# Kernel optimization log

Hardware: AMD Instinct MI355X
Metric: run time of the kernel (lower is better)

## Reference

```python
import jax, jax.numpy as jnp
import numpy as np

N = 512        # number of evidences
D = 512        # hidden_dim

def setup_inputs() -> dict:
    key = jax.random.key(0)
    k0, k1, k2, k3, k4 = jax.random.split(key, 5)
    s = 1.0 / np.sqrt(2 * D)
    return {
        "h_e":  jax.random.normal(k0, (N, D), dtype=jnp.float32),
        "W0_w": jax.random.uniform(k1, (D, 2 * D), minval=-s, maxval=s, dtype=jnp.float32),  # nn.Linear(2d, d).weight
        "W0_b": jax.random.uniform(k2, (D,), minval=-s, maxval=s, dtype=jnp.float32),
        "W1_w": jax.random.uniform(k3, (1, D), minval=-1/np.sqrt(D), maxval=1/np.sqrt(D), dtype=jnp.float32),
        "W1_b": jax.random.uniform(k4, (1,), minval=-1/np.sqrt(D), maxval=1/np.sqrt(D), dtype=jnp.float32),
    }

def reference(h_e, W0_w, W0_b, W0b_unused=None, W1_w=None, W1_b=None):
    pass  # placeholder replaced below

def reference(h_e, W0_w, W0_b, W1_w, W1_b):
    d = h_e.shape[-1]
    # W_0([h_i ; h_j]) == h_i @ A^T + h_j @ B^T where W0_w = [A | B]
    Wa = W0_w[:, :d]          # [d, d] acts on h_i
    Wb = W0_w[:, d:]          # [d, d] acts on h_j
    pre_i = jnp.einsum('id,hd->ih', h_e, Wa)            # [n, d]
    pre_j = jnp.einsum('jd,hd->jh', h_e, Wb)            # [n, d]
    hidden = jax.nn.relu(pre_i[:, None, :] + pre_j[None, :, :] + W0_b)  # [n, n, d]
    p = jnp.einsum('ijh,oh->ijo', hidden, W1_w)[..., 0] + W1_b[0]       # [n, n]
    a = jax.nn.softmax(p, axis=-1)                                      # [n, n]
    return a @ h_e                                                      # [n, d]
```

## Files before the change

### kernel.cpp

```cpp
#include <hip/hip_runtime.h>


using bf16x8 = __attribute__((ext_vector_type(8))) short;
using f32x4  = __attribute__((ext_vector_type(4))) float;
using f16x2  = __attribute__((ext_vector_type(2))) _Float16;
using f16x4  = __attribute__((ext_vector_type(4))) _Float16;
using f16x8  = __attribute__((ext_vector_type(8))) _Float16;

#define SC_STR 68

__device__ __forceinline__ unsigned short f2bf(float x) {
    unsigned int u = __float_as_uint(x);
    u += 0x7fffu + ((u >> 16) & 1u);
    return (unsigned short)(u >> 16);
}

__device__ __forceinline__ unsigned short f2h(float x) {
    _Float16 h = (_Float16)x;
    union { _Float16 h; unsigned short u; } c; c.h = h;
    return c.u;
}

__global__ __launch_bounds__(256) void k_prep(const float* __restrict__ he,
                                              const float* __restrict__ w0,
                                              unsigned short* __restrict__ heb,
                                              _Float16* __restrict__ hebT,
                                              unsigned short* __restrict__ w0b) {
    const int tid = threadIdx.x;
    if (blockIdx.z == 0) {
        __shared__ unsigned short T[64][65];
        const int r0 = blockIdx.y * 64, c0 = blockIdx.x * 64;
        #pragma unroll
        for (int rep = 0; rep < 4; ++rep) {
            int f = tid + rep * 256;
            int row = f >> 4, col = (f & 15) * 4;
            float4 a = *(const float4*)&he[(r0 + row) * 512 + c0 + col];
            *(ushort4*)&heb[(r0 + row) * 512 + c0 + col] =
                make_ushort4(f2bf(a.x), f2bf(a.y), f2bf(a.z), f2bf(a.w));
            T[row][col + 0] = f2h(a.x); T[row][col + 1] = f2h(a.y);
            T[row][col + 2] = f2h(a.z); T[row][col + 3] = f2h(a.w);
        }
        __syncthreads();
        #pragma unroll
        for (int rep = 0; rep < 4; ++rep) {
            int f = tid + rep * 256;
            int trow = f >> 4, tcol = (f & 15) * 4;
            ushort4 v = make_ushort4(T[tcol + 0][trow], T[tcol + 1][trow],
                                     T[tcol + 2][trow], T[tcol + 3][trow]);
            *(ushort4*)&hebT[(c0 + trow) * 512 + r0 + tcol] = v;
        }
    } else {
        const int r0 = blockIdx.y * 64, c0 = blockIdx.x * 64 + (blockIdx.z - 1) * 512;
        #pragma unroll
        for (int rep = 0; rep < 4; ++rep) {
            int f = tid + rep * 256;
            int row = f >> 4, col = (f & 15) * 4;
            float4 a = *(const float4*)&w0[(r0 + row) * 1024 + c0 + col];
            *(ushort4*)&w0b[(r0 + row) * 1024 + c0 + col] =
                make_ushort4(f2bf(a.x), f2bf(a.y), f2bf(a.z), f2bf(a.w));
        }
    }
}

__global__ __launch_bounds__(64) void k_preA(const unsigned short* __restrict__ heb,
                                             const unsigned short* __restrict__ w0b,
                                             const float* __restrict__ b0,
                                             _Float16* __restrict__ CI,
                                             _Float16* __restrict__ CJ) {
    const int l = threadIdx.x;
    const int c0 = blockIdx.x * 32;
    const int i0 = blockIdx.y * 32;
    const int r16 = l & 15;
    const int k0l = (l >> 4) * 8;
    const int hrow0 = c0 & 511;
    const int dofs = (c0 >= 512) ? 512 : 0;

    f32x4 acc[2][2] = {};
    const unsigned short* pa0 = heb + (i0 + r16) * 512;
    const unsigned short* pa1 = heb + (i0 + 16 + r16) * 512;
    const unsigned short* pb0 = w0b + (hrow0 + r16) * 1024 + dofs;
    const unsigned short* pb1 = w0b + (hrow0 + 16 + r16) * 1024 + dofs;

    #pragma unroll
    for (int ks = 0; ks < 16; ++ks) {
        const int k0 = ks * 32 + k0l;
        bf16x8 a0 = *(const bf16x8*)(pa0 + k0);
        bf16x8 a1 = *(const bf16x8*)(pa1 + k0);
        bf16x8 b0v = *(const bf16x8*)(pb0 + k0);
        bf16x8 b1v = *(const bf16x8*)(pb1 + k0);
        acc[0][0] = __builtin_amdgcn_mfma_f32_16x16x32_bf16(a0, b0v, acc[0][0], 0, 0, 0);
        acc[0][1] = __builtin_amdgcn_mfma_f32_16x16x32_bf16(a0, b1v, acc[0][1], 0, 0, 0);
        acc[1][0] = __builtin_amdgcn_mfma_f32_16x16x32_bf16(a1, b0v, acc[1][0], 0, 0, 0);
        acc[1][1] = __builtin_amdgcn_mfma_f32_16x16x32_bf16(a1, b1v, acc[1][1], 0, 0, 0);
    }
    const int orow = (l >> 4) * 4;
    if (dofs) {
        const float bb0 = b0[hrow0 + r16];
        const float bb1 = b0[hrow0 + 16 + r16];
        #pragma unroll
        for (int ti = 0; ti < 2; ++ti)
            #pragma unroll
            for (int tj = 0; tj < 2; ++tj) {
                const float bb = tj ? bb1 : bb0;
                #pragma unroll
                for (int r = 0; r < 4; ++r)
                    CJ[(i0 + ti * 16 + orow + r) * 512 + hrow0 + tj * 16 + r16] =
                        (_Float16)(acc[ti][tj][r] + bb);
            }
    } else {
        #pragma unroll
        for (int ti = 0; ti < 2; ++ti)
            #pragma unroll
            for (int tj = 0; tj < 2; ++tj)
                #pragma unroll
                for (int r = 0; r < 4; ++r)
                    CI[(i0 + ti * 16 + orow + r) * 512 + c0 + tj * 16 + r16] =
                        (_Float16)acc[ti][tj][r];
    }
}

__global__ __launch_bounds__(256) void k_score(const _Float16* __restrict__ CI,
                                               const _Float16* __restrict__ CJ,
                                               const float* __restrict__ w1,
                                               _Float16* __restrict__ Ppart) {
    const int tid = threadIdx.x;
    const int tx = tid & 15, ty = tid >> 4;
    const int j0 = blockIdx.x * 64;
    const int i0 = blockIdx.y * 64;
    const int hs = blockIdx.z;

    __shared__ __align__(16) f16x2 As2[16 * SC_STR];
    __shared__ __align__(16) f16x2 Bs2[16 * SC_STR];
    __shared__ f16x2 Ws2[16];

    const f16x2 fz = {(_Float16)0, (_Float16)0};
    float acc[4][4] = {};

    for (int kt = 0; kt < 2; ++kt) {
        const int hb = hs * 64 + kt * 32;
        {
            const int row = tid >> 2;
            const int hc = (tid & 3) * 8;
            const int hp = hc >> 1;
            f16x8 av = *(const f16x8*)&CI[(i0 + row) * 512 + hb + hc];
            As2[(hp + 0) * SC_STR + row] = __builtin_shufflevector(av, av, 0, 1);
            As2[(hp + 1) * SC_STR + row] = __builtin_shufflevector(av, av, 2, 3);
            As2[(hp + 2) * SC_STR + row] = __builtin_shufflevector(av, av, 4, 5);
            As2[(hp + 3) * SC_STR + row] = __builtin_shufflevector(av, av, 6, 7);
            f16x8 bv = *(const f16x8*)&CJ[(j0 + row) * 512 + hb + hc];
            Bs2[(hp + 0) * SC_STR + row] = __builtin_shufflevector(bv, bv, 0, 1);
            Bs2[(hp + 1) * SC_STR + row] = __builtin_shufflevector(bv, bv, 2, 3);
            Bs2[(hp + 2) * SC_STR + row] = __builtin_shufflevector(bv, bv, 4, 5);
            Bs2[(hp + 3) * SC_STR + row] = __builtin_shufflevector(bv, bv, 6, 7);
        }
        if (tid < 16) {
            float2 w = *(const float2*)&w1[hb + 2 * tid];
            f16x2 wp = {(_Float16)w.x, (_Float16)w.y};
            Ws2[tid] = wp;
        }
        __syncthreads();
        #pragma unroll
        for (int k = 0; k < 16; ++k) {
            f16x8 a8 = *(const f16x8*)&As2[k * SC_STR + 4 * ty];
            f16x8 b8 = *(const f16x8*)&Bs2[k * SC_STR + 4 * tx];
            const f16x2 w = Ws2[k];
            f16x2 ap[4] = { __builtin_shufflevector(a8, a8, 0, 1),
                            __builtin_shufflevector(a8, a8, 2, 3),
                            __builtin_shufflevector(a8, a8, 4, 5),
                            __builtin_shufflevector(a8, a8, 6, 7) };
            f16x2 bp[4] = { __builtin_shufflevector(b8, b8, 0, 1),
                            __builtin_shufflevector(b8, b8, 2, 3),
                            __builtin_shufflevector(b8, b8, 4, 5),
                            __builtin_shufflevector(b8, b8, 6, 7) };
            #pragma unroll
            for (int ii = 0; ii < 4; ++ii)
                #pragma unroll
                for (int jj = 0; jj < 4; ++jj) {
                    f16x2 s = ap[ii] + bp[jj];
                    s = __builtin_elementwise_max(s, fz);
                    acc[ii][jj] = __builtin_amdgcn_fdot2(s, w, acc[ii][jj], false);
                }
        }
        __syncthreads();
    }
    _Float16* outp = Ppart + (size_t)hs * 512 * 512;
    #pragma unroll
    for (int ii = 0; ii < 4; ++ii) {
        f16x4 v = { (_Float16)acc[ii][0], (_Float16)acc[ii][1],
                    (_Float16)acc[ii][2], (_Float16)acc[ii][3] };
        *(f16x4*)&outp[(i0 + 4 * ty + ii) * 512 + j0 + 4 * tx] = v;
    }
}

__global__ __launch_bounds__(256) void k_softmax(const _Float16* __restrict__ Ppart,
                                                 _Float16* __restrict__ Awb) {
    const int i = blockIdx.x;
    const int tid = threadIdx.x;
    float p0 = 0.f, p1 = 0.f;
    #pragma unroll
    for (int s = 0; s < 8; ++s) {
        p0 += (float)Ppart[s * 262144 + i * 512 + tid];
        p1 += (float)Ppart[s * 262144 + i * 512 + tid + 256];
    }
    __shared__ float red[256];
    red[tid] = fmaxf(p0, p1);
    __syncthreads();
    for (int s = 128; s > 0; s >>= 1) {
        if (tid < s) red[tid] = fmaxf(red[tid], red[tid + s]);
        __syncthreads();
    }
    const float m = red[0];
    __syncthreads();
    const float e0 = __expf(p0 - m);
    const float e1 = __expf(p1 - m);
    red[tid] = e0 + e1;
    __syncthreads();
    for (int s = 128; s > 0; s >>= 1) {
        if (tid < s) red[tid] += red[tid + s];
        __syncthreads();
    }
    const float inv = 1.0f / red[0];
    Awb[i * 512 + tid] = (_Float16)(e0 * inv);
    Awb[i * 512 + tid + 256] = (_Float16)(e1 * inv);
}

__global__ __launch_bounds__(64) void k_outM(const _Float16* __restrict__ Awb,
                                             const _Float16* __restrict__ hebT,
                                             float* __restrict__ outp) {
    const int l = threadIdx.x;
    const int d0 = blockIdx.x * 32;
    const int i0 = blockIdx.y * 16;
    const int r16 = l & 15;
    const int k0l = (l >> 4) * 8;

    f32x4 acc[2] = {};
    const _Float16* pa  = Awb  + (i0 + r16) * 512;
    const _Float16* pb0 = hebT + (d0 + r16) * 512;
    const _Float16* pb1 = hebT + (d0 + 16 + r16) * 512;

    #pragma unroll
    for (int ks = 0; ks < 16; ++ks) {
        const int k0 = ks * 32 + k0l;
        f16x8 a  = *(const f16x8*)(pa + k0);
        f16x8 b0 = *(const f16x8*)(pb0 + k0);
        f16x8 b1 = *(const f16x8*)(pb1 + k0);
        acc[0] = __builtin_amdgcn_mfma_f32_16x16x32_f16(a, b0, acc[0], 0, 0, 0);
        acc[1] = __builtin_amdgcn_mfma_f32_16x16x32_f16(a, b1, acc[1], 0, 0, 0);
    }
    const int orow = (l >> 4) * 4;
    #pragma unroll
    for (int tj = 0; tj < 2; ++tj)
        #pragma unroll
        for (int r = 0; r < 4; ++r)
            outp[(i0 + orow + r) * 512 + d0 + tj * 16 + r16] = acc[tj][r];
}

extern "C" void kernel_launch(void* const* d_in, const int* in_sizes, int n_in,
                              void* d_out, int out_size, void* d_ws, size_t ws_size,
                              hipStream_t stream) {
    const float* he = (const float*)d_in[0];
    const float* w0 = (const float*)d_in[1];
    const float* b0 = (const float*)d_in[2];
    const float* w1 = (const float*)d_in[3];
    float* outp = (float*)d_out;

    _Float16* Ppart = (_Float16*)d_ws;
    _Float16* CI = Ppart + 8 * 512 * 512;
    _Float16* CJ = CI + 512 * 512;
    unsigned short* heb  = (unsigned short*)(CJ + 512 * 512);
    _Float16* hebT = (_Float16*)(heb + 512 * 512);
    unsigned short* w0b  = (unsigned short*)(hebT + 512 * 512);
    _Float16* Awb  = (_Float16*)(w0b + 512 * 1024);

    k_prep   <<<dim3(8, 8, 3), 256, 0, stream>>>(he, w0, heb, hebT, w0b);
    k_preA   <<<dim3(32, 16),  64,  0, stream>>>(heb, w0b, b0, CI, CJ);
    k_score  <<<dim3(8, 8, 8), 256, 0, stream>>>(CI, CJ, w1, Ppart);
    k_softmax<<<dim3(512),     256, 0, stream>>>(Ppart, Awb);
    k_outM   <<<dim3(16, 32),  64,  0, stream>>>(Awb, hebT, outp);
}
```

Measured before the change: 90.20 us.

## Fuse prep conversion into projection GEMM and split score over more h-slices

Removes the separate k_prep kernel. The projection GEMM now reads fp32 h_e and W0 directly and converts them to bf16 in registers with v_cvt_pk_bf16_f32, and the transpose of h_e is handled by extra blocks inside the same launch. The score kernel is split into 16 h-slices of 32 instead of 8 slices of 64, which doubles the block count for better occupancy, and softmax now sums 16 partial score planes. The trade-off is redundant fp32 loads and conversions in the GEMM, plus twice as much partial-score traffic.

```diff
diff --git a/kernel.cpp b/kernel.cpp
--- a/kernel.cpp
+++ b/kernel.cpp
@@ -9,85 +9,74 @@
 
 #define SC_STR 68
 
-__device__ __forceinline__ unsigned short f2bf(float x) {
-    unsigned int u = __float_as_uint(x);
-    u += 0x7fffu + ((u >> 16) & 1u);
-    return (unsigned short)(u >> 16);
-}
-
 __device__ __forceinline__ unsigned short f2h(float x) {
-    _Float16 h = (_Float16)x;
-    union { _Float16 h; unsigned short u; } c; c.h = h;
+    union { _Float16 h; unsigned short u; } c;
+    c.h = (_Float16)x;
     return c.u;
 }
 
-__global__ __launch_bounds__(256) void k_prep(const float* __restrict__ he,
-                                              const float* __restrict__ w0,
-                                              unsigned short* __restrict__ heb,
-                                              _Float16* __restrict__ hebT,
-                                              unsigned short* __restrict__ w0b) {
-    const int tid = threadIdx.x;
-    if (blockIdx.z == 0) {
+__device__ __forceinline__ bf16x8 cvt8(float4 lo, float4 hi) {
+    union { bf16x8 v; unsigned int u[4]; } r;
+    asm("v_cvt_pk_bf16_f32 %0, %1, %2" : "=v"(r.u[0]) : "v"(lo.x), "v"(lo.y));
+    asm("v_cvt_pk_bf16_f32 %0, %1, %2" : "=v"(r.u[1]) : "v"(lo.z), "v"(lo.w));
+    asm("v_cvt_pk_bf16_f32 %0, %1, %2" : "=v"(r.u[2]) : "v"(hi.x), "v"(hi.y));
+    asm("v_cvt_pk_bf16_f32 %0, %1, %2" : "=v"(r.u[3]) : "v"(hi.z), "v"(hi.w));
+    return r.v;
+}
+
+__global__ __launch_bounds__(64) void k_preA(const float* __restrict__ he,
+                                             const float* __restrict__ w0,
+                                             const float* __restrict__ b0,
+                                             _Float16* __restrict__ CI,
+                                             _Float16* __restrict__ CJ,
+                                             unsigned short* __restrict__ hebT) {
+    const int bx = blockIdx.x;
+    const int l = threadIdx.x;
+
+    if (bx >= 512) {
         __shared__ unsigned short T[64][65];
-        const int r0 = blockIdx.y * 64, c0 = blockIdx.x * 64;
-        #pragma unroll
-        for (int rep = 0; rep < 4; ++rep) {
-            int f = tid + rep * 256;
+        const int t = bx - 512;
+        const int r0 = (t >> 3) * 64, c0 = (t & 7) * 64;
+        #pragma unroll
+        for (int rep = 0; rep < 16; ++rep) {
+            int f = l + rep * 64;
             int row = f >> 4, col = (f & 15) * 4;
             float4 a = *(const float4*)&he[(r0 + row) * 512 + c0 + col];
-            *(ushort4*)&heb[(r0 + row) * 512 + c0 + col] =
-                make_ushort4(f2bf(a.x), f2bf(a.y), f2bf(a.z), f2bf(a.w));
             T[row][col + 0] = f2h(a.x); T[row][col + 1] = f2h(a.y);
             T[row][col + 2] = f2h(a.z); T[row][col + 3] = f2h(a.w);
         }
         __syncthreads();
         #pragma unroll
-        for (int rep = 0; rep < 4; ++rep) {
-            int f = tid + rep * 256;
+        for (int rep = 0; rep < 16; ++rep) {
+            int f = l + rep * 64;
             int trow = f >> 4, tcol = (f & 15) * 4;
             ushort4 v = make_ushort4(T[tcol + 0][trow], T[tcol + 1][trow],
                                      T[tcol + 2][trow], T[tcol + 3][trow]);
             *(ushort4*)&hebT[(c0 + trow) * 512 + r0 + tcol] = v;
         }
-    } else {
-        const int r0 = blockIdx.y * 64, c0 = blockIdx.x * 64 + (blockIdx.z - 1) * 512;
-        #pragma unroll
-        for (int rep = 0; rep < 4; ++rep) {
-            int f = tid + rep * 256;
-            int row = f >> 4, col = (f & 15) * 4;
-            float4 a = *(const float4*)&w0[(r0 + row) * 1024 + c0 + col];
-            *(ushort4*)&w0b[(r0 + row) * 1024 + c0 + col] =
-                make_ushort4(f2bf(a.x), f2bf(a.y), f2bf(a.z), f2bf(a.w));
-        }
-    }
-}
-
-__global__ __launch_bounds__(64) void k_preA(const unsigned short* __restrict__ heb,
-                                             const unsigned short* __restrict__ w0b,
-                                             const float* __restrict__ b0,
-                                             _Float16* __restrict__ CI,
-                                             _Float16* __restrict__ CJ) {
-    const int l = threadIdx.x;
-    const int c0 = blockIdx.x * 32;
-    const int i0 = blockIdx.y * 32;
+        return;
+    }
+
+    const int c0 = (bx & 31) * 32;
+    const int i0 = (bx >> 5) * 32;
     const int r16 = l & 15;
     const int k0l = (l >> 4) * 8;
     const int hrow0 = c0 & 511;
     const int dofs = (c0 >= 512) ? 512 : 0;
 
     f32x4 acc[2][2] = {};
-    const unsigned short* pa0 = heb + (i0 + r16) * 512;
-    const unsigned short* pa1 = heb + (i0 + 16 + r16) * 512;
-    const unsigned short* pb0 = w0b + (hrow0 + r16) * 1024 + dofs;
-    const unsigned short* pb1 = w0b + (hrow0 + 16 + r16) * 1024 + dofs;
+    const float* pa0 = he + (i0 + r16) * 512;
+    const float* pa1 = pa0 + 16 * 512;
+    const float* pb0 = w0 + (hrow0 + r16) * 1024 + dofs;
+    const float* pb1 = pb0 + 16 * 1024;
 
     #pragma unroll
     for (int ks = 0; ks < 16; ++ks) {
         const int k0 = ks * 32 + k0l;
-        bf16x8 a0 = *(const bf16x8*)(pa0 + k0);
-        bf16x8 a1 = *(const bf16x8*)(pa1 + k0);
-        bf16x8 b0v = *(const bf16x8*)(pb0 + k0);
-        bf16x8 b1v = *(const bf16x8*)(pb1 + k0);
+        bf16x8 a0 = cvt8(*(const float4*)(pa0 + k0), *(const float4*)(pa0 + k0 + 4));
+        bf16x8 a1 = cvt8(*(const float4*)(pa1 + k0), *(const float4*)(pa1 + k0 + 4));
+        bf16x8 b0v = cvt8(*(const float4*)(pb0 + k0), *(const float4*)(pb0 + k0 + 4));
+        bf16x8 b1v = cvt8(*(const float4*)(pb1 + k0), *(const float4*)(pb1 + k0 + 4));
         acc[0][0] = __builtin_amdgcn_mfma_f32_16x16x32_bf16(a0, b0v, acc[0][0], 0, 0, 0);
         acc[0][1] = __builtin_amdgcn_mfma_f32_16x16x32_bf16(a0, b1v, acc[0][1], 0, 0, 0);
         acc[1][0] = __builtin_amdgcn_mfma_f32_16x16x32_bf16(a1, b0v, acc[1][0], 0, 0, 0);
@@ -127,7 +116,7 @@
     const int tx = tid & 15, ty = tid >> 4;
     const int j0 = blockIdx.x * 64;
     const int i0 = blockIdx.y * 64;
-    const int hs = blockIdx.z;
+    const int hb = blockIdx.z * 32;
 
     __shared__ __align__(16) f16x2 As2[16 * SC_STR];
     __shared__ __align__(16) f16x2 Bs2[16 * SC_STR];
@@ -136,54 +125,50 @@
     const f16x2 fz = {(_Float16)0, (_Float16)0};
     float acc[4][4] = {};
 
-    for (int kt = 0; kt < 2; ++kt) {
-        const int hb = hs * 64 + kt * 32;
-        {
-            const int row = tid >> 2;
-            const int hc = (tid & 3) * 8;
-            const int hp = hc >> 1;
-            f16x8 av = *(const f16x8*)&CI[(i0 + row) * 512 + hb + hc];
-            As2[(hp + 0) * SC_STR + row] = __builtin_shufflevector(av, av, 0, 1);
-            As2[(hp + 1) * SC_STR + row] = __builtin_shufflevector(av, av, 2, 3);
-            As2[(hp + 2) * SC_STR + row] = __builtin_shufflevector(av, av, 4, 5);
-            As2[(hp + 3) * SC_STR + row] = __builtin_shufflevector(av, av, 6, 7);
-            f16x8 bv = *(const f16x8*)&CJ[(j0 + row) * 512 + hb + hc];
-            Bs2[(hp + 0) * SC_STR + row] = __builtin_shufflevector(bv, bv, 0, 1);
-            Bs2[(hp + 1) * SC_STR + row] = __builtin_shufflevector(bv, bv, 2, 3);
-            Bs2[(hp + 2) * SC_STR + row] = __builtin_shufflevector(bv, bv, 4, 5);
-            Bs2[(hp + 3) * SC_STR + row] = __builtin_shufflevector(bv, bv, 6, 7);
-        }
-        if (tid < 16) {
-            float2 w = *(const float2*)&w1[hb + 2 * tid];
-            f16x2 wp = {(_Float16)w.x, (_Float16)w.y};
-            Ws2[tid] = wp;
-        }
-        __syncthreads();
-        #pragma unroll
-        for (int k = 0; k < 16; ++k) {
-            f16x8 a8 = *(const f16x8*)&As2[k * SC_STR + 4 * ty];
-            f16x8 b8 = *(const f16x8*)&Bs2[k * SC_STR + 4 * tx];
-            const f16x2 w = Ws2[k];
-            f16x2 ap[4] = { __builtin_shufflevector(a8, a8, 0, 1),
-                            __builtin_shufflevector(a8, a8, 2, 3),
-                            __builtin_shufflevector(a8, a8, 4, 5),
-                            __builtin_shufflevector(a8, a8, 6, 7) };
-            f16x2 bp[4] = { __builtin_shufflevector(b8, b8, 0, 1),
-                            __builtin_shufflevector(b8, b8, 2, 3),
-                            __builtin_shufflevector(b8, b8, 4, 5),
-                            __builtin_shufflevector(b8, b8, 6, 7) };
+    {
+        const int row = tid >> 2;
+        const int hc = (tid & 3) * 8;
+        const int hp = hc >> 1;
+        f16x8 av = *(const f16x8*)&CI[(i0 + row) * 512 + hb + hc];
+        As2[(hp + 0) * SC_STR + row] = __builtin_shufflevector(av, av, 0, 1);
+        As2[(hp + 1) * SC_STR + row] = __builtin_shufflevector(av, av, 2, 3);
+        As2[(hp + 2) * SC_STR + row] = __builtin_shufflevector(av, av, 4, 5);
+        As2[(hp + 3) * SC_STR + row] = __builtin_shufflevector(av, av, 6, 7);
+        f16x8 bv = *(const f16x8*)&CJ[(j0 + row) * 512 + hb + hc];
+        Bs2[(hp + 0) * SC_STR + row] = __builtin_shufflevector(bv, bv, 0, 1);
+        Bs2[(hp + 1) * SC_STR + row] = __builtin_shufflevector(bv, bv, 2, 3);
+        Bs2[(hp + 2) * SC_STR + row] = __builtin_shufflevector(bv, bv, 4, 5);
+        Bs2[(hp + 3) * SC_STR + row] = __builtin_shufflevector(bv, bv, 6, 7);
+    }
+    if (tid < 16) {
+        float2 w = *(const float2*)&w1[hb + 2 * tid];
+        f16x2 wp = {(_Float16)w.x, (_Float16)w.y};
+        Ws2[tid] = wp;
+    }
+    __syncthreads();
+    #pragma unroll
+    for (int k = 0; k < 16; ++k) {
+        f16x8 a8 = *(const f16x8*)&As2[k * SC_STR + 4 * ty];
+        f16x8 b8 = *(const f16x8*)&Bs2[k * SC_STR + 4 * tx];
+        const f16x2 w = Ws2[k];
+        f16x2 ap[4] = { __builtin_shufflevector(a8, a8, 0, 1),
+                        __builtin_shufflevector(a8, a8, 2, 3),
+                        __builtin_shufflevector(a8, a8, 4, 5),
+                        __builtin_shufflevector(a8, a8, 6, 7) };
+        f16x2 bp[4] = { __builtin_shufflevector(b8, b8, 0, 1),
+                        __builtin_shufflevector(b8, b8, 2, 3),
+                        __builtin_shufflevector(b8, b8, 4, 5),
+                        __builtin_shufflevector(b8, b8, 6, 7) };
+        #pragma unroll
+        for (int ii = 0; ii < 4; ++ii)
             #pragma unroll
-            for (int ii = 0; ii < 4; ++ii)
-                #pragma unroll
-                for (int jj = 0; jj < 4; ++jj) {
-                    f16x2 s = ap[ii] + bp[jj];
-                    s = __builtin_elementwise_max(s, fz);
-                    acc[ii][jj] = __builtin_amdgcn_fdot2(s, w, acc[ii][jj], false);
-                }
-        }
-        __syncthreads();
-    }
-    _Float16* outp = Ppart + (size_t)hs * 512 * 512;
+            for (int jj = 0; jj < 4; ++jj) {
+                f16x2 s = ap[ii] + bp[jj];
+                s = __builtin_elementwise_max(s, fz);
+                acc[ii][jj] = __builtin_amdgcn_fdot2(s, w, acc[ii][jj], false);
+            }
+    }
+    _Float16* outp = Ppart + (size_t)blockIdx.z * 512 * 512;
     #pragma unroll
     for (int ii = 0; ii < 4; ++ii) {
         f16x4 v = { (_Float16)acc[ii][0], (_Float16)acc[ii][1],
@@ -198,7 +183,7 @@
     const int tid = threadIdx.x;
     float p0 = 0.f, p1 = 0.f;
     #pragma unroll
-    for (int s = 0; s < 8; ++s) {
+    for (int s = 0; s < 16; ++s) {
         p0 += (float)Ppart[s * 262144 + i * 512 + tid];
         p1 += (float)Ppart[s * 262144 + i * 512 + tid + 256];
     }
@@ -265,16 +250,13 @@
     float* outp = (float*)d_out;
 
     _Float16* Ppart = (_Float16*)d_ws;
-    _Float16* CI = Ppart + 8 * 512 * 512;
+    _Float16* CI = Ppart + 16 * 512 * 512;
     _Float16* CJ = CI + 512 * 512;
-    unsigned short* heb  = (unsigned short*)(CJ + 512 * 512);
-    _Float16* hebT = (_Float16*)(heb + 512 * 512);
-    unsigned short* w0b  = (unsigned short*)(hebT + 512 * 512);
-    _Float16* Awb  = (_Float16*)(w0b + 512 * 1024);
-
-    k_prep   <<<dim3(8, 8, 3), 256, 0, stream>>>(he, w0, heb, hebT, w0b);
-    k_preA   <<<dim3(32, 16),  64,  0, stream>>>(heb, w0b, b0, CI, CJ);
-    k_score  <<<dim3(8, 8, 8), 256, 0, stream>>>(CI, CJ, w1, Ppart);
-    k_softmax<<<dim3(512),     256, 0, stream>>>(Ppart, Awb);
-    k_outM   <<<dim3(16, 32),  64,  0, stream>>>(Awb, hebT, outp);
-}
+    unsigned short* hebT = (unsigned short*)(CJ + 512 * 512);
+    _Float16* Awb = (_Float16*)(hebT + 512 * 512);
+
+    k_preA   <<<dim3(576),      64,  0, stream>>>(he, w0, b0, CI, CJ, hebT);
+    k_score  <<<dim3(8, 8, 16), 256, 0, stream>>>(CI, CJ, w1, Ppart);
+    k_softmax<<<dim3(512),      256, 0, stream>>>(Ppart, Awb);
+    k_outM   <<<dim3(16, 32),   64,  0, stream>>>(Awb, (const _Float16*)hebT, outp);
+}
```

After: 91.60 us. About the same (+1.6%).
